# Kernel optimization log

Measured on AMD Instinct MI355X. Metric: run time of the kernel, lower is better.

The kernel has to match this reference:

```python
import jax, jax.numpy as jnp
import numpy as np

N_HEADS = 16
EMBED_DIM = 2048
BATCH, SEQ = 2, 2048


def setup_inputs() -> dict:
    key = jax.random.key(0)
    k1, k2, k3, k4, k5 = jax.random.split(key, 5)
    s_in = 1.0 / np.sqrt(EMBED_DIM)
    return {
        "x": jax.random.normal(k1, (BATCH, SEQ, EMBED_DIM), dtype=jnp.float32),
        "w_in": jax.random.normal(k2, (3 * EMBED_DIM, EMBED_DIM), dtype=jnp.float32) * s_in,
        "b_in": jax.random.normal(k3, (3 * EMBED_DIM,), dtype=jnp.float32) * 0.02,
        "w_out": jax.random.normal(k4, (EMBED_DIM, EMBED_DIM), dtype=jnp.float32) * s_in,
        "b_out": jax.random.normal(k5, (EMBED_DIM,), dtype=jnp.float32) * 0.02,
        "causal_mask": 1,
    }


def reference(x, w_in, b_in, w_out, b_out, causal_mask):
    b, l, e = x.shape
    h, d = N_HEADS, e // N_HEADS
    qkv = x @ w_in.T + b_in                      # [b, l, 3e]
    q, k, v = jnp.split(qkv, 3, axis=-1)
    # b l (h d) -> b h l d
    q = q.reshape(b, l, h, d).transpose(0, 2, 1, 3)
    k = k.reshape(b, l, h, d).transpose(0, 2, 1, 3)
    v = v.reshape(b, l, h, d).transpose(0, 2, 1, 3)
    scores = jnp.einsum("bhqd,bhkd->bhqk", q, k) / jnp.sqrt(jnp.float32(d))
    if causal_mask:
        tri = jnp.triu(jnp.ones((l, l), dtype=bool), k=1)  # True above diagonal
        scores = jnp.where(tri, -jnp.inf, scores)
    attn = jax.nn.softmax(scores, axis=-1)
    out = jnp.einsum("bhqk,bhkd->bhqd", attn, v)  # [b, h, l, d]
    out = out.transpose(0, 2, 1, 3).reshape(b, l, e)
    return out @ w_out.T + b_out
```

## Files before the change

kernel.cpp:

```cpp
#include <hip/hip_runtime.h>
#include <hip/hip_bf16.h>
#include <math.h>

typedef __attribute__((ext_vector_type(4))) float floatx4;
typedef __attribute__((ext_vector_type(16))) float floatx16;
typedef __attribute__((ext_vector_type(8))) __bf16 bf16x8;

__device__ __forceinline__ unsigned short f2bf(float f) {
    union { float f; unsigned int u; } v; v.f = f;
    unsigned int u = v.u;
    u += 0x7FFFu + ((u >> 16) & 1u);
    return (unsigned short)(u >> 16);
}

__device__ __forceinline__ unsigned int pkbf(float a, float b) {
    return (unsigned int)f2bf(a) | ((unsigned int)f2bf(b) << 16);
}

__device__ __forceinline__ void gl_lds16(const void* g, void* l) {
    __builtin_amdgcn_global_load_lds(
        (const __attribute__((address_space(1))) void*)g,
        (__attribute__((address_space(3))) void*)l, 16, 0, 0);
}

__global__ void cast_f32_bf16(const float* __restrict__ in,
                              unsigned short* __restrict__ out, int n) {
    int i = (blockIdx.x * blockDim.x + threadIdx.x) * 4;
    if (i + 4 <= n) {
        float4 f = *(const float4*)(in + i);
        ushort4 o;
        o.x = f2bf(f.x); o.y = f2bf(f.y); o.z = f2bf(f.z); o.w = f2bf(f.w);
        *(ushort4*)(out + i) = o;
    }
}


#define VMCNT(n) asm volatile("s_waitcnt vmcnt(" #n ")" ::: "memory")
#define BARF()   do { __builtin_amdgcn_s_barrier(); asm volatile("" ::: "memory"); } while (0)

#define STAGE_A(bsel, tt, h) do { \
    const unsigned short* _s = Ab + (size_t)((h) * 128 + rstage) * K + (tt) * 64 + scol; \
    char* _d = bufc + (bsel) * 65536 + (h) * 16384 + wid * 1024; \
    gl_lds16(_s, _d); \
    gl_lds16(_s + (size_t)64 * K, _d + 8192); \
} while (0)

#define STAGE_B(bsel, tt, h) do { \
    const unsigned short* _s = Bb + (size_t)((h) * 128 + rstage) * K + (tt) * 64 + scol; \
    char* _d = bufc + (bsel) * 65536 + 32768 + (h) * 16384 + wid * 1024; \
    gl_lds16(_s, _d); \
    gl_lds16(_s + (size_t)64 * K, _d + 8192); \
} while (0)

#define RDA(base, ii, kse) (*(const bf16x8*)((base) + (ii) * 2048 + rdoffA + (kse)))
#define RDB(base, jj, kse) (*(const bf16x8*)((base) + (jj) * 2048 + rdoffB + (kse)))

#define MFMA_Q(iofs, jofs, BV) do { \
    __builtin_amdgcn_s_setprio(1); \
    _Pragma("unroll") \
    for (int ii = 0; ii < 4; ++ii) { \
        _Pragma("unroll") \
        for (int jj = 0; jj < 2; ++jj) { \
            acc[(iofs) + ii][(jofs) + jj] = __builtin_amdgcn_mfma_f32_16x16x32_bf16( \
                aF[ii * 2 + 0], BV[jj * 2 + 0], acc[(iofs) + ii][(jofs) + jj], 0, 0, 0); \
            acc[(iofs) + ii][(jofs) + jj] = __builtin_amdgcn_mfma_f32_16x16x32_bf16( \
                aF[ii * 2 + 1], BV[jj * 2 + 1], acc[(iofs) + ii][(jofs) + jj], 0, 0, 0); \
        } } \
    __builtin_amdgcn_s_setprio(0); \
} while (0)

template<int MODE>
__global__ __launch_bounds__(512, 2) void gemm8p(
    const unsigned short* __restrict__ A,
    const unsigned short* __restrict__ B,
    const float* __restrict__ bias,
    float* __restrict__ Cf,
    unsigned short* __restrict__ q_ws,
    unsigned short* __restrict__ k_ws,
    unsigned short* __restrict__ vT_ws,
    int M, int N, int K)
{
    extern __shared__ char ldsc[];
    char* const bufc = ldsc;

    const int nby = M >> 8;
    const int nwg = gridDim.x;
    const int qq = nwg >> 3;
    const int wg = (blockIdx.x & 7) * qq + (blockIdx.x >> 3);
    const int by = wg % nby, bx = wg / nby;
    const int m0 = by << 8, n0 = bx << 8;

    const int tid = threadIdx.x;
    const int lane = tid & 63, wid = tid >> 6;
    const int li = lane & 15, quad = lane >> 4;
    const int wr = wid >> 2, wc = wid & 3;

    const int rstage = tid >> 3;
    const int scol = (((tid & 7) ^ ((tid >> 3) & 7)) << 3);
    const unsigned short* Ab = A + (size_t)m0 * K;
    const unsigned short* Bb = B + (size_t)n0 * K;

    const int swz = (lane & 7) << 4;
    const int ks0 = ((quad << 4)     ) ^ swz;
    const int ks1 = ((quad << 4) + 64) ^ swz;
    const int rdoffA = li * 128;
    const int rdoffB = li * 128 + ((wc & 1) << 13);

    const char* rdA0 = bufc + wr * 16384;
    const char* rdB0 = bufc + 32768 + (wc >> 1) * 16384;
    const char* rdA1 = rdA0 + 65536;
    const char* rdB1 = rdB0 + 65536;

    floatx4 acc[8][4] = {};
    bf16x8 aF[8], bL[4], bH[4];

    const int KTn = K >> 6;

    STAGE_A(0, 0, 0); STAGE_A(0, 0, 1); STAGE_B(0, 0, 0); STAGE_B(0, 0, 1);
    STAGE_B(1, 1, 0); STAGE_B(1, 1, 1); STAGE_A(1, 1, 0);
    VMCNT(6);
    BARF();

    for (int t = 0; t < KTn; t += 2) {
        const bool pf = (t + 2 < KTn);

        #pragma unroll
        for (int ii = 0; ii < 4; ++ii) { aF[ii*2+0] = RDA(rdA0, ii, ks0); aF[ii*2+1] = RDA(rdA0, ii, ks1); }
        #pragma unroll
        for (int jj = 0; jj < 2; ++jj) { bL[jj*2+0] = RDB(rdB0, jj, ks0); bL[jj*2+1] = RDB(rdB0, jj, ks1); }
        STAGE_A(1, t + 1, 1);
        BARF();
        MFMA_Q(0, 0, bL);
        BARF();

        #pragma unroll
        for (int jj = 0; jj < 2; ++jj) { bH[jj*2+0] = RDB(rdB0, 2 + jj, ks0); bH[jj*2+1] = RDB(rdB0, 2 + jj, ks1); }
        BARF();
        MFMA_Q(0, 2, bH);
        BARF();

        #pragma unroll
        for (int ii = 0; ii < 4; ++ii) { aF[ii*2+0] = RDA(rdA0, 4 + ii, ks0); aF[ii*2+1] = RDA(rdA0, 4 + ii, ks1); }
        if (pf) STAGE_B(0, t + 2, 0);
        BARF();
        MFMA_Q(4, 0, bL);
        BARF();

        if (pf) { STAGE_B(0, t + 2, 1); STAGE_A(0, t + 2, 0); }
        BARF();
        MFMA_Q(4, 2, bH);
        if (pf) { VMCNT(6); } else { VMCNT(0); }
        BARF();

        #pragma unroll
        for (int ii = 0; ii < 4; ++ii) { aF[ii*2+0] = RDA(rdA1, ii, ks0); aF[ii*2+1] = RDA(rdA1, ii, ks1); }
        #pragma unroll
        for (int jj = 0; jj < 2; ++jj) { bL[jj*2+0] = RDB(rdB1, jj, ks0); bL[jj*2+1] = RDB(rdB1, jj, ks1); }
        if (pf) STAGE_A(0, t + 2, 1);
        BARF();
        MFMA_Q(0, 0, bL);
        BARF();

        #pragma unroll
        for (int jj = 0; jj < 2; ++jj) { bH[jj*2+0] = RDB(rdB1, 2 + jj, ks0); bH[jj*2+1] = RDB(rdB1, 2 + jj, ks1); }
        BARF();
        MFMA_Q(0, 2, bH);
        BARF();

        #pragma unroll
        for (int ii = 0; ii < 4; ++ii) { aF[ii*2+0] = RDA(rdA1, 4 + ii, ks0); aF[ii*2+1] = RDA(rdA1, 4 + ii, ks1); }
        if (pf) STAGE_B(1, t + 3, 0);
        BARF();
        MFMA_Q(4, 0, bL);
        BARF();

        if (pf) { STAGE_B(1, t + 3, 1); STAGE_A(1, t + 3, 0); }
        BARF();
        MFMA_Q(4, 2, bH);
        VMCNT(6);
        BARF();
    }

    const int colb = n0 + wc * 64;
    const int rowb = m0 + wr * 128;
    if (MODE == 0) {
        #pragma unroll
        for (int i2 = 0; i2 < 8; ++i2)
            #pragma unroll
            for (int j2 = 0; j2 < 4; ++j2) {
                const int col = colb + j2 * 16 + li;
                const float bv = bias[col];
                #pragma unroll
                for (int r = 0; r < 4; ++r) {
                    const int row = rowb + i2 * 16 + quad * 4 + r;
                    Cf[(size_t)row * N + col] = acc[i2][j2][r] + bv;
                }
            }
    } else {
        const int bb = m0 >> 11;
        const int which = n0 >> 11;
        #pragma unroll
        for (int i2 = 0; i2 < 8; ++i2)
            #pragma unroll
            for (int j2 = 0; j2 < 4; ++j2) {
                const int ng = colb + j2 * 16 + li;
                const float bv = bias[ng];
                const int e = ng & 2047, hh = e >> 7, dd = e & 127;
                const size_t bh = (size_t)(bb * 16 + hh);
                const int l0 = (rowb + i2 * 16 + quad * 4) & 2047;
                if (which == 2) {
                    ushort4 o4;
                    o4.x = f2bf(acc[i2][j2][0] + bv);
                    o4.y = f2bf(acc[i2][j2][1] + bv);
                    o4.z = f2bf(acc[i2][j2][2] + bv);
                    o4.w = f2bf(acc[i2][j2][3] + bv);
                    *(ushort4*)(vT_ws + (bh * 128 + dd) * 2048 + l0) = o4;
                } else {
                    unsigned short* dst = (which == 0) ? q_ws : k_ws;
                    #pragma unroll
                    for (int r = 0; r < 4; ++r)
                        dst[(bh * 2048 + (l0 + r)) * 128 + dd] = f2bf(acc[i2][j2][r] + bv);
                }
            }
    }
}

#define AP 8
__global__ __launch_bounds__(256, 2) void attn_kernel(
    const unsigned short* __restrict__ q_ws,
    const unsigned short* __restrict__ k_ws,
    const unsigned short* __restrict__ vT_ws,
    unsigned short* __restrict__ aout,
    const int* __restrict__ causal_ptr)
{
    __shared__ unsigned short Ksm[128][128 + AP];
    __shared__ unsigned short Vsm[128][128 + AP];

    const int ord = blockIdx.x;
    int qt, bhid;
    if (ord < 256) { qt = ord >> 5;              bhid = ord & 31; }
    else           { qt = 15 - ((ord - 256) >> 5); bhid = ord & 31; }
    const int b = bhid >> 4, h = bhid & 15;

    const int tid = threadIdx.x;
    const int lane = tid & 63, w = tid >> 6;
    const int lq = lane & 31;
    const int half = lane >> 5;
    const size_t bh = (size_t)(b * 16 + h);
    const unsigned short* Qp = q_ws + bh * 2048 * 128;
    const unsigned short* Kp = k_ws + bh * 2048 * 128;
    const unsigned short* Vp = vT_ws + bh * 128 * 2048;
    const int causal = causal_ptr[0];
    const float scale = 0.08838834764831845f;

    const int qg = qt * 128 + w * 32 + lq;
    bf16x8 qf[8];
    #pragma unroll
    for (int s = 0; s < 8; ++s)
        qf[s] = *(const bf16x8*)(Qp + (size_t)qg * 128 + s * 16 + half * 8);

    floatx16 O[4] = {};
    float m_i = -INFINITY, l_i = 0.f;

    const int myEnd = causal ? qt : 15;
    for (int kt = 0; kt <= myEnd; ++kt) {
        #pragma unroll
        for (int c = 0; c < 8; ++c) {
            int chunk = c * 256 + tid;
            int row = chunk >> 4;
            int cc  = (chunk & 15) * 8;
            *(uint4*)(&Ksm[row][cc]) =
                *(const uint4*)(Kp + (size_t)(kt * 128 + row) * 128 + cc);
            *(uint4*)(&Vsm[row][cc]) =
                *(const uint4*)(Vp + (size_t)row * 2048 + kt * 128 + cc);
        }
        __syncthreads();

        floatx16 S[4] = {};
        #pragma unroll
        for (int ct = 0; ct < 4; ++ct)
            #pragma unroll
            for (int s = 0; s < 8; ++s) {
                bf16x8 kf = *(const bf16x8*)(&Ksm[ct * 32 + lq][s * 16 + half * 8]);
                S[ct] = __builtin_amdgcn_mfma_f32_32x32x16_bf16(kf, qf[s], S[ct], 0, 0, 0);
            }

        const bool diag = causal && (kt == qt);
        float mx = -INFINITY;
        #pragma unroll
        for (int ct = 0; ct < 4; ++ct)
            #pragma unroll
            for (int r = 0; r < 16; ++r) {
                float sv = S[ct][r] * scale;
                if (diag) {
                    int key = 32 * ct + (r & 3) + 8 * (r >> 2) + 4 * half;
                    if (kt * 128 + key > qg) sv = -INFINITY;
                }
                S[ct][r] = sv;
                mx = fmaxf(mx, sv);
            }
        mx = fmaxf(mx, __shfl_xor(mx, 32, 64));
        float m_new = fmaxf(m_i, mx);
        float m_use = (m_new == -INFINITY) ? 0.f : m_new;
        float alpha = __expf(m_i - m_use);

        float rs = 0.f;
        #pragma unroll
        for (int ct = 0; ct < 4; ++ct)
            #pragma unroll
            for (int r = 0; r < 16; ++r) {
                float p = __expf(S[ct][r] - m_use);
                S[ct][r] = p;
                rs += p;
            }
        rs += __shfl_xor(rs, 32, 64);
        l_i = l_i * alpha + rs;
        m_i = m_new;
        #pragma unroll
        for (int dt = 0; dt < 4; ++dt)
            #pragma unroll
            for (int r = 0; r < 16; ++r)
                O[dt][r] *= alpha;

        bf16x8 pfr[8];
        #pragma unroll
        for (int ct = 0; ct < 4; ++ct)
            #pragma unroll
            for (int h2 = 0; h2 < 2; ++h2) {
                int base = 8 * h2;
                unsigned int pk0 = pkbf(S[ct][base + 0], S[ct][base + 1]);
                unsigned int pk1 = pkbf(S[ct][base + 2], S[ct][base + 3]);
                unsigned int pk2 = pkbf(S[ct][base + 4], S[ct][base + 5]);
                unsigned int pk3 = pkbf(S[ct][base + 6], S[ct][base + 7]);
                unsigned int x0 = __shfl_xor((int)pk0, 32, 64);
                unsigned int x1 = __shfl_xor((int)pk1, 32, 64);
                unsigned int x2 = __shfl_xor((int)pk2, 32, 64);
                unsigned int x3 = __shfl_xor((int)pk3, 32, 64);
                union { unsigned int u[4]; bf16x8 v; } fr;
                fr.u[0] = half ? x2 : pk0;
                fr.u[1] = half ? x3 : pk1;
                fr.u[2] = half ? pk2 : x0;
                fr.u[3] = half ? pk3 : x1;
                pfr[ct * 2 + h2] = fr.v;
            }

        #pragma unroll
        for (int dt = 0; dt < 4; ++dt)
            #pragma unroll
            for (int s = 0; s < 8; ++s) {
                bf16x8 vf = *(const bf16x8*)(&Vsm[dt * 32 + lq][s * 16 + half * 8]);
                O[dt] = __builtin_amdgcn_mfma_f32_32x32x16_bf16(vf, pfr[s], O[dt], 0, 0, 0);
            }
        __syncthreads();
    }

    const float invl = 1.0f / l_i;
    #pragma unroll
    for (int dt = 0; dt < 4; ++dt)
        #pragma unroll
        for (int g = 0; g < 4; ++g) {
            int dbase = dt * 32 + g * 8 + half * 4;
            ushort4 o4;
            o4.x = f2bf(O[dt][g * 4 + 0] * invl);
            o4.y = f2bf(O[dt][g * 4 + 1] * invl);
            o4.z = f2bf(O[dt][g * 4 + 2] * invl);
            o4.w = f2bf(O[dt][g * 4 + 3] * invl);
            *(ushort4*)(&Ksm[w * 32 + lq][dbase]) = o4;
        }
    __syncthreads();
    #pragma unroll
    for (int c = 0; c < 8; ++c) {
        int chunk = c * 256 + tid;
        int row = chunk >> 4;
        int dc = (chunk & 15) * 8;
        uint4 v = *(const uint4*)(&Ksm[row][dc]);
        *(uint4*)(aout + ((size_t)b * 2048 + qt * 128 + row) * 2048 + h * 128 + dc) = v;
    }
}

extern "C" void kernel_launch(void* const* d_in, const int* in_sizes, int n_in,
                              void* d_out, int out_size, void* d_ws, size_t ws_size,
                              hipStream_t stream) {
    const float* x     = (const float*)d_in[0];
    const float* w_in  = (const float*)d_in[1];
    const float* b_in  = (const float*)d_in[2];
    const float* w_out = (const float*)d_in[3];
    const float* b_out = (const float*)d_in[4];
    const int* causal  = (const int*)d_in[5];

    char* ws = (char*)d_ws;
    unsigned short* xb    = (unsigned short*)ws; ws += (size_t)4096 * 2048 * 2;
    unsigned short* wb    = (unsigned short*)ws; ws += (size_t)6144 * 2048 * 2;
    unsigned short* wob   = (unsigned short*)ws; ws += (size_t)2048 * 2048 * 2;
    unsigned short* q_ws  = (unsigned short*)ws; ws += (size_t)32 * 2048 * 128 * 2;
    unsigned short* k_ws  = (unsigned short*)ws; ws += (size_t)32 * 2048 * 128 * 2;
    unsigned short* vT_ws = (unsigned short*)ws; ws += (size_t)32 * 2048 * 128 * 2;
    unsigned short* aout  = (unsigned short*)ws; ws += (size_t)4096 * 2048 * 2;

    static int once = []() {
        auto* f0 = gemm8p<0>;
        auto* f1 = gemm8p<1>;
        hipFuncSetAttribute((const void*)f0,
            hipFuncAttributeMaxDynamicSharedMemorySize, 131072);
        hipFuncSetAttribute((const void*)f1,
            hipFuncAttributeMaxDynamicSharedMemorySize, 131072);
        return 0;
    }();
    (void)once;

    cast_f32_bf16<<<8192, 256, 0, stream>>>(x, xb, 4096 * 2048);
    cast_f32_bf16<<<12288, 256, 0, stream>>>(w_in, wb, 6144 * 2048);
    cast_f32_bf16<<<4096, 256, 0, stream>>>(w_out, wob, 2048 * 2048);

    gemm8p<1><<<384, 512, 131072, stream>>>(
        xb, wb, b_in, nullptr, q_ws, k_ws, vT_ws, 4096, 6144, 2048);

    attn_kernel<<<512, 256, 0, stream>>>(
        q_ws, k_ws, vT_ws, aout, causal);

    gemm8p<0><<<128, 512, 131072, stream>>>(
        aout, wob, b_out, (float*)d_out, nullptr, nullptr, nullptr,
        4096, 2048, 2048);
}
```

Baseline: 394.4 us.

## Shrink GEMM tile to 256x128 and stage QKV epilogue through LDS

Changes the GEMM block tile from 256x256 to 256x128 and doubles the grid for both projections. This is meant to improve wave balance on 256 CUs, since the output GEMM previously launched only 128 blocks. The K loop is restructured: each warp now loads all 8 A fragments at once and runs two MFMA chunks per k-tile, with whole-tile staging and fewer barriers. The QKV epilogue now writes Q/K and transposed V through an LDS buffer, giving coalesced 16-byte global stores instead of scattered 2-byte ones. The cost is lower arithmetic intensity per block, more A-tile reloads from global memory, and higher register pressure from 16 A fragments.

```diff
diff --git a/kernel.cpp b/kernel.cpp
--- a/kernel.cpp
+++ b/kernel.cpp
@@ -36,41 +36,47 @@
 
 
 #define VMCNT(n) asm volatile("s_waitcnt vmcnt(" #n ")" ::: "memory")
-#define BARF()   do { __builtin_amdgcn_s_barrier(); asm volatile("" ::: "memory"); } while (0)
-
-#define STAGE_A(bsel, tt, h) do { \
+#define LGKM0()  asm volatile("s_waitcnt lgkmcnt(0)" ::: "memory")
+#define BARF()   do { asm volatile("" ::: "memory"); __builtin_amdgcn_s_barrier(); \
+                      asm volatile("" ::: "memory"); } while (0)
+
+#define STAGE_A4(bsel, tt, h) do { \
     const unsigned short* _s = Ab + (size_t)((h) * 128 + rstage) * K + (tt) * 64 + scol; \
-    char* _d = bufc + (bsel) * 65536 + (h) * 16384 + wid * 1024; \
+    char* _d = bufc + (bsel) * 49152 + (h) * 16384 + wid * 1024; \
     gl_lds16(_s, _d); \
     gl_lds16(_s + (size_t)64 * K, _d + 8192); \
 } while (0)
 
-#define STAGE_B(bsel, tt, h) do { \
-    const unsigned short* _s = Bb + (size_t)((h) * 128 + rstage) * K + (tt) * 64 + scol; \
-    char* _d = bufc + (bsel) * 65536 + 32768 + (h) * 16384 + wid * 1024; \
+#define STAGE_B4(bsel, tt, h) do { \
+    const unsigned short* _s = Bb + (size_t)((h) * 64 + rstage) * K + (tt) * 64 + scol; \
+    char* _d = bufc + (bsel) * 49152 + 32768 + (h) * 8192 + wid * 1024; \
     gl_lds16(_s, _d); \
-    gl_lds16(_s + (size_t)64 * K, _d + 8192); \
+} while (0)
+
+#define STAGE_TILE(bsel, tt) do { \
+    STAGE_A4(bsel, tt, 0); STAGE_A4(bsel, tt, 1); \
+    STAGE_B4(bsel, tt, 0); STAGE_B4(bsel, tt, 1); \
 } while (0)
 
 #define RDA(base, ii, kse) (*(const bf16x8*)((base) + (ii) * 2048 + rdoffA + (kse)))
 #define RDB(base, jj, kse) (*(const bf16x8*)((base) + (jj) * 2048 + rdoffB + (kse)))
 
-#define MFMA_Q(iofs, jofs, BV) do { \
+#define MFMA_C(iofs) do { \
     __builtin_amdgcn_s_setprio(1); \
     _Pragma("unroll") \
     for (int ii = 0; ii < 4; ++ii) { \
         _Pragma("unroll") \
         for (int jj = 0; jj < 2; ++jj) { \
-            acc[(iofs) + ii][(jofs) + jj] = __builtin_amdgcn_mfma_f32_16x16x32_bf16( \
-                aF[ii * 2 + 0], BV[jj * 2 + 0], acc[(iofs) + ii][(jofs) + jj], 0, 0, 0); \
-            acc[(iofs) + ii][(jofs) + jj] = __builtin_amdgcn_mfma_f32_16x16x32_bf16( \
-                aF[ii * 2 + 1], BV[jj * 2 + 1], acc[(iofs) + ii][(jofs) + jj], 0, 0, 0); \
+            acc[(iofs) + ii][jj] = __builtin_amdgcn_mfma_f32_16x16x32_bf16( \
+                aF[((iofs) + ii) * 2 + 0], bL[jj * 2 + 0], acc[(iofs) + ii][jj], 0, 0, 0); \
+            acc[(iofs) + ii][jj] = __builtin_amdgcn_mfma_f32_16x16x32_bf16( \
+                aF[((iofs) + ii) * 2 + 1], bL[jj * 2 + 1], acc[(iofs) + ii][jj], 0, 0, 0); \
         } } \
     __builtin_amdgcn_s_setprio(0); \
 } while (0)
 
 template<int MODE>
-__global__ __launch_bounds__(512, 2) void gemm8p(
+__global__ __launch_bounds__(512, 2) void gemm4p(
     const unsigned short* __restrict__ A,
     const unsigned short* __restrict__ B,
     const float* __restrict__ bias,
@@ -88,7 +94,7 @@
     const int qq = nwg >> 3;
     const int wg = (blockIdx.x & 7) * qq + (blockIdx.x >> 3);
     const int by = wg % nby, bx = wg / nby;
-    const int m0 = by << 8, n0 = bx << 8;
+    const int m0 = by << 8, n0 = bx << 7;
 
     const int tid = threadIdx.x;
     const int lane = tid & 63, wid = tid >> 6;
@@ -104,20 +110,20 @@
     const int ks0 = ((quad << 4)     ) ^ swz;
     const int ks1 = ((quad << 4) + 64) ^ swz;
     const int rdoffA = li * 128;
-    const int rdoffB = li * 128 + ((wc & 1) << 13);
+    const int rdoffB = li * 128 + ((wc & 1) << 12);
 
     const char* rdA0 = bufc + wr * 16384;
-    const char* rdB0 = bufc + 32768 + (wc >> 1) * 16384;
-    const char* rdA1 = rdA0 + 65536;
-    const char* rdB1 = rdB0 + 65536;
-
-    floatx4 acc[8][4] = {};
-    bf16x8 aF[8], bL[4], bH[4];
+    const char* rdB0 = bufc + 32768 + (wc >> 1) * 8192;
+    const char* rdA1 = rdA0 + 49152;
+    const char* rdB1 = rdB0 + 49152;
+
+    floatx4 acc[8][2] = {};
+    bf16x8 aF[16], bL[4];
 
     const int KTn = K >> 6;
 
-    STAGE_A(0, 0, 0); STAGE_A(0, 0, 1); STAGE_B(0, 0, 0); STAGE_B(0, 0, 1);
-    STAGE_B(1, 1, 0); STAGE_B(1, 1, 1); STAGE_A(1, 1, 0);
+    STAGE_TILE(0, 0);
+    STAGE_TILE(1, 1);
     VMCNT(6);
     BARF();
 
@@ -125,103 +131,104 @@
         const bool pf = (t + 2 < KTn);
 
         #pragma unroll
-        for (int ii = 0; ii < 4; ++ii) { aF[ii*2+0] = RDA(rdA0, ii, ks0); aF[ii*2+1] = RDA(rdA0, ii, ks1); }
+        for (int ii = 0; ii < 8; ++ii) { aF[ii*2+0] = RDA(rdA0, ii, ks0); aF[ii*2+1] = RDA(rdA0, ii, ks1); }
         #pragma unroll
         for (int jj = 0; jj < 2; ++jj) { bL[jj*2+0] = RDB(rdB0, jj, ks0); bL[jj*2+1] = RDB(rdB0, jj, ks1); }
-        STAGE_A(1, t + 1, 1);
-        BARF();
-        MFMA_Q(0, 0, bL);
-        BARF();
-
-        #pragma unroll
-        for (int jj = 0; jj < 2; ++jj) { bH[jj*2+0] = RDB(rdB0, 2 + jj, ks0); bH[jj*2+1] = RDB(rdB0, 2 + jj, ks1); }
-        BARF();
-        MFMA_Q(0, 2, bH);
-        BARF();
-
-        #pragma unroll
-        for (int ii = 0; ii < 4; ++ii) { aF[ii*2+0] = RDA(rdA0, 4 + ii, ks0); aF[ii*2+1] = RDA(rdA0, 4 + ii, ks1); }
-        if (pf) STAGE_B(0, t + 2, 0);
-        BARF();
-        MFMA_Q(4, 0, bL);
-        BARF();
-
-        if (pf) { STAGE_B(0, t + 2, 1); STAGE_A(0, t + 2, 0); }
-        BARF();
-        MFMA_Q(4, 2, bH);
+        BARF();
+        MFMA_C(0);
+        LGKM0();
+        BARF();
+
+        if (pf) STAGE_TILE(0, t + 2);
+        BARF();
+        MFMA_C(4);
         if (pf) { VMCNT(6); } else { VMCNT(0); }
         BARF();
 
         #pragma unroll
-        for (int ii = 0; ii < 4; ++ii) { aF[ii*2+0] = RDA(rdA1, ii, ks0); aF[ii*2+1] = RDA(rdA1, ii, ks1); }
+        for (int ii = 0; ii < 8; ++ii) { aF[ii*2+0] = RDA(rdA1, ii, ks0); aF[ii*2+1] = RDA(rdA1, ii, ks1); }
         #pragma unroll
         for (int jj = 0; jj < 2; ++jj) { bL[jj*2+0] = RDB(rdB1, jj, ks0); bL[jj*2+1] = RDB(rdB1, jj, ks1); }
-        if (pf) STAGE_A(0, t + 2, 1);
-        BARF();
-        MFMA_Q(0, 0, bL);
-        BARF();
-
-        #pragma unroll
-        for (int jj = 0; jj < 2; ++jj) { bH[jj*2+0] = RDB(rdB1, 2 + jj, ks0); bH[jj*2+1] = RDB(rdB1, 2 + jj, ks1); }
-        BARF();
-        MFMA_Q(0, 2, bH);
-        BARF();
-
-        #pragma unroll
-        for (int ii = 0; ii < 4; ++ii) { aF[ii*2+0] = RDA(rdA1, 4 + ii, ks0); aF[ii*2+1] = RDA(rdA1, 4 + ii, ks1); }
-        if (pf) STAGE_B(1, t + 3, 0);
-        BARF();
-        MFMA_Q(4, 0, bL);
-        BARF();
-
-        if (pf) { STAGE_B(1, t + 3, 1); STAGE_A(1, t + 3, 0); }
-        BARF();
-        MFMA_Q(4, 2, bH);
-        VMCNT(6);
+        BARF();
+        MFMA_C(0);
+        LGKM0();
+        BARF();
+
+        if (pf) STAGE_TILE(1, t + 3);
+        BARF();
+        MFMA_C(4);
+        if (pf) { VMCNT(6); } else { VMCNT(0); }
         BARF();
     }
 
-    const int colb = n0 + wc * 64;
-    const int rowb = m0 + wr * 128;
+    const int colb = wc * 32;
+    const int rowb = wr * 128;
     if (MODE == 0) {
         #pragma unroll
         for (int i2 = 0; i2 < 8; ++i2)
             #pragma unroll
-            for (int j2 = 0; j2 < 4; ++j2) {
-                const int col = colb + j2 * 16 + li;
+            for (int j2 = 0; j2 < 2; ++j2) {
+                const int col = n0 + colb + j2 * 16 + li;
                 const float bv = bias[col];
                 #pragma unroll
                 for (int r = 0; r < 4; ++r) {
-                    const int row = rowb + i2 * 16 + quad * 4 + r;
+                    const int row = m0 + rowb + i2 * 16 + quad * 4 + r;
                     Cf[(size_t)row * N + col] = acc[i2][j2][r] + bv;
                 }
             }
     } else {
-        const int bb = m0 >> 11;
-        const int which = n0 >> 11;
-        #pragma unroll
-        for (int i2 = 0; i2 < 8; ++i2)
-            #pragma unroll
-            for (int j2 = 0; j2 < 4; ++j2) {
-                const int ng = colb + j2 * 16 + li;
-                const float bv = bias[ng];
-                const int e = ng & 2047, hh = e >> 7, dd = e & 127;
-                const size_t bh = (size_t)(bb * 16 + hh);
-                const int l0 = (rowb + i2 * 16 + quad * 4) & 2047;
-                if (which == 2) {
-                    ushort4 o4;
-                    o4.x = f2bf(acc[i2][j2][0] + bv);
-                    o4.y = f2bf(acc[i2][j2][1] + bv);
-                    o4.z = f2bf(acc[i2][j2][2] + bv);
-                    o4.w = f2bf(acc[i2][j2][3] + bv);
-                    *(ushort4*)(vT_ws + (bh * 128 + dd) * 2048 + l0) = o4;
-                } else {
-                    unsigned short* dst = (which == 0) ? q_ws : k_ws;
+        const int which = bx >> 4;
+        const int hh = bx & 15;
+        const int lbase = m0 & 2047;
+        const size_t bh = (size_t)((m0 >> 11) * 16 + hh);
+        if (which == 2) {
+            unsigned short (*Lv)[264] = (unsigned short(*)[264])ldsc;
+            #pragma unroll
+            for (int i2 = 0; i2 < 8; ++i2)
+                #pragma unroll
+                for (int j2 = 0; j2 < 2; ++j2) {
+                    const int col = colb + j2 * 16 + li;
+                    const float bv = bias[n0 + col];
                     #pragma unroll
-                    for (int r = 0; r < 4; ++r)
-                        dst[(bh * 2048 + (l0 + r)) * 128 + dd] = f2bf(acc[i2][j2][r] + bv);
+                    for (int r = 0; r < 4; ++r) {
+                        const int row = rowb + i2 * 16 + quad * 4 + r;
+                        Lv[col][row] = f2bf(acc[i2][j2][r] + bv);
+                    }
                 }
-            }
+            __syncthreads();
+            #pragma unroll
+            for (int c = 0; c < 8; ++c) {
+                int chunk = c * 512 + tid;
+                int d = chunk >> 5;
+                int ls = (chunk & 31) * 8;
+                *(uint4*)(vT_ws + (bh * 128 + d) * 2048 + lbase + ls) =
+                    *(const uint4*)&Lv[d][ls];
+            }
+        } else {
+            unsigned short (*Lq)[136] = (unsigned short(*)[136])ldsc;
+            #pragma unroll
+            for (int i2 = 0; i2 < 8; ++i2)
+                #pragma unroll
+                for (int j2 = 0; j2 < 2; ++j2) {
+                    const int col = colb + j2 * 16 + li;
+                    const float bv = bias[n0 + col];
+                    #pragma unroll
+                    for (int r = 0; r < 4; ++r) {
+                        const int row = rowb + i2 * 16 + quad * 4 + r;
+                        Lq[row][col] = f2bf(acc[i2][j2][r] + bv);
+                    }
+                }
+            __syncthreads();
+            unsigned short* dst = which ? k_ws : q_ws;
+            #pragma unroll
+            for (int c = 0; c < 8; ++c) {
+                int chunk = c * 512 + tid;
+                int row = chunk >> 4;
+                int dc = (chunk & 15) * 8;
+                *(uint4*)(dst + (bh * 2048 + lbase + row) * (size_t)128 + dc) =
+                    *(const uint4*)&Lq[row][dc];
+            }
+        }
     }
 }
 
@@ -398,12 +405,12 @@
     unsigned short* aout  = (unsigned short*)ws; ws += (size_t)4096 * 2048 * 2;
 
     static int once = []() {
-        auto* f0 = gemm8p<0>;
-        auto* f1 = gemm8p<1>;
+        auto* f0 = gemm4p<0>;
+        auto* f1 = gemm4p<1>;
         hipFuncSetAttribute((const void*)f0,
-            hipFuncAttributeMaxDynamicSharedMemorySize, 131072);
+            hipFuncAttributeMaxDynamicSharedMemorySize, 98304);
         hipFuncSetAttribute((const void*)f1,
-            hipFuncAttributeMaxDynamicSharedMemorySize, 131072);
+            hipFuncAttributeMaxDynamicSharedMemorySize, 98304);
         return 0;
     }();
     (void)once;
@@ -412,13 +419,13 @@
     cast_f32_bf16<<<12288, 256, 0, stream>>>(w_in, wb, 6144 * 2048);
     cast_f32_bf16<<<4096, 256, 0, stream>>>(w_out, wob, 2048 * 2048);
 
-    gemm8p<1><<<384, 512, 131072, stream>>>(
+    gemm4p<1><<<768, 512, 98304, stream>>>(
         xb, wb, b_in, nullptr, q_ws, k_ws, vT_ws, 4096, 6144, 2048);
 
     attn_kernel<<<512, 256, 0, stream>>>(
         q_ws, k_ws, vT_ws, aout, causal);
 
-    gemm8p<0><<<128, 512, 131072, stream>>>(
+    gemm4p<0><<<256, 512, 98304, stream>>>(
         aout, wob, b_out, (float*)d_out, nullptr, nullptr, nullptr,
         4096, 2048, 2048);
 }
```

New measurement: 383.4 us. -2.8%, faster.
